# Kernel optimization log

Measured on AMD Instinct MI355X. Metric: run time of the kernel, lower is better.

Reference implementation:

```python
import jax, jax.numpy as jnp
import numpy as np

S, B, I, H, O = 512, 256, 64, 512, 25

def setup_inputs() -> dict:
    key = jax.random.key(0)
    ks = jax.random.split(key, 7)
    k = 1.0 / np.sqrt(H)  # torch nn.RNN / nn.Linear default init bound
    x = jax.random.normal(ks[0], (S, B, I), dtype=jnp.float32)
    W_ih = jax.random.uniform(ks[1], (H, I), jnp.float32, -k, k)
    W_hh = jax.random.uniform(ks[2], (H, H), jnp.float32, -k, k)
    b_ih = jax.random.uniform(ks[3], (H,), jnp.float32, -k, k)
    b_hh = jax.random.uniform(ks[4], (H,), jnp.float32, -k, k)
    W2 = jax.random.uniform(ks[5], (O, H), jnp.float32, -k, k)
    b2 = jax.random.uniform(ks[6], (O,), jnp.float32, -k, k)
    return {"x": x, "W_ih": W_ih, "W_hh": W_hh, "b_ih": b_ih, "b_hh": b_hh, "W2": W2, "b2": b2}

def reference(x, W_ih, W_hh, b_ih, b_hh, W2, b2):
    # Precompute input projection for all timesteps in one big GEMM: (S,B,H)
    xi = jnp.einsum('sbi,hi->sbh', x, W_ih) + b_ih
    h0 = jnp.zeros((x.shape[1], W_hh.shape[0]), dtype=x.dtype)
    W_hh_T = W_hh.T
    def step(h_prev, xi_t):
        h = jax.nn.relu(xi_t + h_prev @ W_hh_T + b_hh)
        return h, h
    _, out = jax.lax.scan(step, h0, xi)  # out: (S, B, H)
    # Faithful to original: out[:, -1, :] selects last batch element -> (S, H)
    y = out[:, -1, :] @ W2.T + b2  # (S, 25)
    return y
```

## Files before the change

### kernel.cpp

```cpp
#include <hip/hip_runtime.h>


#define S_ 512
#define B_ 256
#define I_ 64
#define H_ 512
#define O_ 25
#define G_ 16
#define R_ 32

__global__ __launch_bounds__(256) void rnn_pre(
    const float* __restrict__ x, const float* __restrict__ W_ih,
    const float* __restrict__ b_ih, const float* __restrict__ b_hh,
    float* __restrict__ xi, unsigned* __restrict__ hg) {
  const int t = blockIdx.x;
  const int tid = threadIdx.x;
  const int o = blockIdx.y * 256 + tid;
  if (t == 0 && blockIdx.y == 0) {
    hg[tid] = 0x80000000u;
    hg[tid + 256] = 0x80000000u;
    hg[tid + 512] = 0x80000000u;
    hg[tid + 768] = 0x80000000u;
  }
  __shared__ float xr[I_];
  if (tid < I_) xr[tid] = x[(t * B_ + (B_ - 1)) * I_ + tid];
  __syncthreads();
  float acc = b_ih[o] + b_hh[o];
  const float4* wp = (const float4*)(W_ih + o * I_);
#pragma unroll
  for (int j = 0; j < I_ / 4; ++j) {
    float4 w4 = wp[j];
    acc += w4.x * xr[4 * j] + w4.y * xr[4 * j + 1] + w4.z * xr[4 * j + 2] +
           w4.w * xr[4 * j + 3];
  }
  xi[t * H_ + o] = acc;
}

__global__ __launch_bounds__(256) void rnn_seq(
    const float* __restrict__ W_hh, const float* __restrict__ xi,
    float* __restrict__ hseq, unsigned* __restrict__ hg) {
  const int tid = threadIdx.x;
  const int b = blockIdx.x;
  const int r = tid & 31;
  const int seg = tid >> 5;
  const int row = b * R_ + r;
  const int k0 = seg * 64;
  const int wave = tid >> 6;
  const int own_lo = b * R_;
  const int own_hi = b * R_ + R_;

  __shared__ float h_l[H_];
  __shared__ float part[4 * R_];

  float w[64];
  {
    const float4* wp = (const float4*)(W_hh + row * H_ + k0);
#pragma unroll
    for (int j = 0; j < 16; ++j) {
      float4 v = wp[j];
      w[4 * j] = v.x; w[4 * j + 1] = v.y; w[4 * j + 2] = v.z; w[4 * j + 3] = v.w;
    }
  }
  for (int n = tid; n < H_; n += 256) h_l[n] = 0.0f;

  float xiv = (tid < R_) ? xi[own_lo + tid] : 0.0f;
  __syncthreads();

  const int n0 = tid, n1 = tid + 256;
  const bool own0 = (n0 >= own_lo && n0 < own_hi);
  const bool own1 = (n1 >= own_lo && n1 < own_hi);

  for (int s = 0; s < S_; ++s) {
    float a0 = 0.f, a1 = 0.f, a2 = 0.f, a3 = 0.f;
    const float4* hp = (const float4*)(h_l + k0);
#pragma unroll
    for (int j = 0; j < 16; ++j) {
      float4 hv = hp[j];
      a0 = fmaf(w[4 * j + 0], hv.x, a0);
      a1 = fmaf(w[4 * j + 1], hv.y, a1);
      a2 = fmaf(w[4 * j + 2], hv.z, a2);
      a3 = fmaf(w[4 * j + 3], hv.w, a3);
    }
    float acc = (a0 + a1) + (a2 + a3);
    acc += __shfl_xor(acc, 32, 64);
    if ((tid & 32) == 0) part[wave * R_ + r] = acc;
    __syncthreads();

    const unsigned phase = (unsigned)((s >> 1) & 1);
    unsigned* buf = hg + (s & 1) * H_;

    if (tid < R_) {
      float sum = part[tid] + part[R_ + tid] + part[2 * R_ + tid] +
                  part[3 * R_ + tid] + xiv;
      float h = fmaxf(sum, 0.0f);
      h_l[own_lo + tid] = h;
      hseq[s * H_ + own_lo + tid] = h;
      __hip_atomic_store(&buf[own_lo + tid],
                         __float_as_uint(h) | (phase << 31),
                         __ATOMIC_RELAXED, __HIP_MEMORY_SCOPE_AGENT);
    }

    if (s == S_ - 1) break;

    if (tid < R_) xiv = xi[(s + 1) * H_ + own_lo + tid];

    bool need0 = !own0, need1 = !own1;
    unsigned p0, p1;
    while (need0 | need1) {
      if (need0)
        p0 = __hip_atomic_load(&buf[n0], __ATOMIC_RELAXED, __HIP_MEMORY_SCOPE_AGENT);
      if (need1)
        p1 = __hip_atomic_load(&buf[n1], __ATOMIC_RELAXED, __HIP_MEMORY_SCOPE_AGENT);
      if (need0 && (p0 >> 31) == phase) {
        h_l[n0] = __uint_as_float(p0 & 0x7fffffffu);
        need0 = false;
      }
      if (need1 && (p1 >> 31) == phase) {
        h_l[n1] = __uint_as_float(p1 & 0x7fffffffu);
        need1 = false;
      }
    }
    __syncthreads();
  }
}

__global__ __launch_bounds__(256) void rnn_post(
    const float* __restrict__ hseq, const float* __restrict__ W2,
    const float* __restrict__ b2, float* __restrict__ y) {
  const int t = blockIdx.x;
  const int tid = threadIdx.x;
  __shared__ float hl[H_];
  __shared__ float part[256];
  for (int n = tid; n < H_; n += 256) hl[n] = hseq[t * H_ + n];
  __syncthreads();
  const int o = tid >> 3;
  const int seg = tid & 7;
  float acc = 0.0f;
  if (o < O_) {
    const float4* wp = (const float4*)(W2 + o * H_ + seg * 64);
    const float4* hp = (const float4*)(hl + seg * 64);
#pragma unroll
    for (int j = 0; j < 16; ++j) {
      float4 w4 = wp[j];
      float4 h4 = hp[j];
      acc += w4.x * h4.x + w4.y * h4.y + w4.z * h4.z + w4.w * h4.w;
    }
  }
  part[tid] = acc;
  __syncthreads();
  if (tid < O_) {
    float sum = 0.0f;
#pragma unroll
    for (int j = 0; j < 8; ++j) sum += part[tid * 8 + j];
    y[t * O_ + tid] = sum + b2[tid];
  }
}

extern "C" void kernel_launch(void* const* d_in, const int* in_sizes, int n_in,
                              void* d_out, int out_size, void* d_ws, size_t ws_size,
                              hipStream_t stream) {
  const float* x    = (const float*)d_in[0];
  const float* W_ih = (const float*)d_in[1];
  const float* W_hh = (const float*)d_in[2];
  const float* b_ih = (const float*)d_in[3];
  const float* b_hh = (const float*)d_in[4];
  const float* W2   = (const float*)d_in[5];
  const float* b2   = (const float*)d_in[6];
  float* y = (float*)d_out;

  float* xi   = (float*)d_ws;
  float* hseq = xi + S_ * H_;
  unsigned* hg = (unsigned*)(hseq + S_ * H_);

  rnn_pre<<<dim3(S_, 2), 256, 0, stream>>>(x, W_ih, b_ih, b_hh, xi, hg);
  rnn_seq<<<G_, 256, 0, stream>>>(W_hh, xi, hseq, hg);
  rnn_post<<<S_, 256, 0, stream>>>(hseq, W2, b2, y);
}
```

Before: 819.6 us.

## Halve sequential RNN blocks, use per-block mailboxes and double-buffered hidden state

Cuts the persistent recurrence kernel from 16 to 8 blocks, each owning 64 rows, with four threads per row reducing through shuffles instead of a shared-memory partial sum plus barrier. Each block now has its own mailbox, and producers push their values to every other block rather than publishing to one shared global buffer. A double-buffered shared hidden state removes one __syncthreads per step. In exchange each thread holds 128 weight registers, which risks spills, and more atomic stores are issued per step.

```diff
diff --git a/kernel.cpp b/kernel.cpp
--- a/kernel.cpp
+++ b/kernel.cpp
@@ -6,21 +6,18 @@
 #define I_ 64
 #define H_ 512
 #define O_ 25
-#define G_ 16
-#define R_ 32
+#define G_ 8
+#define R_ 64
 
 __global__ __launch_bounds__(256) void rnn_pre(
     const float* __restrict__ x, const float* __restrict__ W_ih,
     const float* __restrict__ b_ih, const float* __restrict__ b_hh,
-    float* __restrict__ xi, unsigned* __restrict__ hg) {
+    float* __restrict__ xi, unsigned* __restrict__ mbox) {
   const int t = blockIdx.x;
   const int tid = threadIdx.x;
   const int o = blockIdx.y * 256 + tid;
   if (t == 0 && blockIdx.y == 0) {
-    hg[tid] = 0x80000000u;
-    hg[tid + 256] = 0x80000000u;
-    hg[tid + 512] = 0x80000000u;
-    hg[tid + 768] = 0x80000000u;
+    for (int j = tid; j < G_ * 2 * H_; j += 256) mbox[j] = 0x80000000u;
   }
   __shared__ float xr[I_];
   if (tid < I_) xr[tid] = x[(t * B_ + (B_ - 1)) * I_ + tid];
@@ -38,43 +35,46 @@
 
 __global__ __launch_bounds__(256) void rnn_seq(
     const float* __restrict__ W_hh, const float* __restrict__ xi,
-    float* __restrict__ hseq, unsigned* __restrict__ hg) {
+    float* __restrict__ hseq, unsigned* __restrict__ mbox) {
   const int tid = threadIdx.x;
   const int b = blockIdx.x;
-  const int r = tid & 31;
-  const int seg = tid >> 5;
-  const int row = b * R_ + r;
-  const int k0 = seg * 64;
-  const int wave = tid >> 6;
+  const int row_l = tid >> 2;
+  const int q = tid & 3;
+  const int row = b * R_ + row_l;
+  const int k0 = q * 128;
   const int own_lo = b * R_;
-  const int own_hi = b * R_ + R_;
 
-  __shared__ float h_l[H_];
-  __shared__ float part[4 * R_];
+  __shared__ float h_l[2][H_];
 
-  float w[64];
+  float w[128];
   {
     const float4* wp = (const float4*)(W_hh + row * H_ + k0);
 #pragma unroll
-    for (int j = 0; j < 16; ++j) {
+    for (int j = 0; j < 32; ++j) {
       float4 v = wp[j];
       w[4 * j] = v.x; w[4 * j + 1] = v.y; w[4 * j + 2] = v.z; w[4 * j + 3] = v.w;
     }
   }
-  for (int n = tid; n < H_; n += 256) h_l[n] = 0.0f;
+  for (int n = tid; n < H_; n += 256) h_l[0][n] = 0.0f;
 
-  float xiv = (tid < R_) ? xi[own_lo + tid] : 0.0f;
+  const bool fin = (q == 0);
+  float xiv = fin ? xi[own_lo + row_l] : 0.0f;
   __syncthreads();
 
   const int n0 = tid, n1 = tid + 256;
-  const bool own0 = (n0 >= own_lo && n0 < own_hi);
-  const bool own1 = (n1 >= own_lo && n1 < own_hi);
+  const bool own0 = (n0 >= own_lo && n0 < own_lo + R_);
+  const bool own1 = (n1 >= own_lo && n1 < own_lo + R_);
+  unsigned* const mb0 = mbox + (b * 2 + 0) * H_;
+  unsigned* const mb1 = mbox + (b * 2 + 1) * H_;
 
   for (int s = 0; s < S_; ++s) {
+    const float* hr = h_l[s & 1];
+    float* hw = h_l[(s + 1) & 1];
+
     float a0 = 0.f, a1 = 0.f, a2 = 0.f, a3 = 0.f;
-    const float4* hp = (const float4*)(h_l + k0);
+    const float4* hp = (const float4*)(hr + k0);
 #pragma unroll
-    for (int j = 0; j < 16; ++j) {
+    for (int j = 0; j < 32; ++j) {
       float4 hv = hp[j];
       a0 = fmaf(w[4 * j + 0], hv.x, a0);
       a1 = fmaf(w[4 * j + 1], hv.y, a1);
@@ -82,28 +82,30 @@
       a3 = fmaf(w[4 * j + 3], hv.w, a3);
     }
     float acc = (a0 + a1) + (a2 + a3);
-    acc += __shfl_xor(acc, 32, 64);
-    if ((tid & 32) == 0) part[wave * R_ + r] = acc;
-    __syncthreads();
+    acc += __shfl_xor(acc, 1, 64);
+    acc += __shfl_xor(acc, 2, 64);
 
     const unsigned phase = (unsigned)((s >> 1) & 1);
-    unsigned* buf = hg + (s & 1) * H_;
+    const int bsel = s & 1;
 
-    if (tid < R_) {
-      float sum = part[tid] + part[R_ + tid] + part[2 * R_ + tid] +
-                  part[3 * R_ + tid] + xiv;
-      float h = fmaxf(sum, 0.0f);
-      h_l[own_lo + tid] = h;
-      hseq[s * H_ + own_lo + tid] = h;
-      __hip_atomic_store(&buf[own_lo + tid],
-                         __float_as_uint(h) | (phase << 31),
-                         __ATOMIC_RELAXED, __HIP_MEMORY_SCOPE_AGENT);
+    if (fin) {
+      float h = fmaxf(acc + xiv, 0.0f);
+      hw[row] = h;
+      hseq[s * H_ + row] = h;
+      unsigned pk = __float_as_uint(h) | (phase << 31);
+#pragma unroll
+      for (int c = 0; c < G_; ++c) {
+        if (c != b)
+          __hip_atomic_store(&mbox[(c * 2 + bsel) * H_ + row], pk,
+                             __ATOMIC_RELAXED, __HIP_MEMORY_SCOPE_AGENT);
+      }
     }
 
     if (s == S_ - 1) break;
 
-    if (tid < R_) xiv = xi[(s + 1) * H_ + own_lo + tid];
+    if (fin) xiv = xi[(s + 1) * H_ + own_lo + row_l];
 
+    unsigned* const buf = bsel ? mb1 : mb0;
     bool need0 = !own0, need1 = !own1;
     unsigned p0, p1;
     while (need0 | need1) {
@@ -112,11 +114,11 @@
       if (need1)
         p1 = __hip_atomic_load(&buf[n1], __ATOMIC_RELAXED, __HIP_MEMORY_SCOPE_AGENT);
       if (need0 && (p0 >> 31) == phase) {
-        h_l[n0] = __uint_as_float(p0 & 0x7fffffffu);
+        hw[n0] = __uint_as_float(p0 & 0x7fffffffu);
         need0 = false;
       }
       if (need1 && (p1 >> 31) == phase) {
-        h_l[n1] = __uint_as_float(p1 & 0x7fffffffu);
+        hw[n1] = __uint_as_float(p1 & 0x7fffffffu);
         need1 = false;
       }
     }
@@ -170,9 +172,9 @@
 
   float* xi   = (float*)d_ws;
   float* hseq = xi + S_ * H_;
-  unsigned* hg = (unsigned*)(hseq + S_ * H_);
+  unsigned* mbox = (unsigned*)(hseq + S_ * H_);
 
-  rnn_pre<<<dim3(S_, 2), 256, 0, stream>>>(x, W_ih, b_ih, b_hh, xi, hg);
-  rnn_seq<<<G_, 256, 0, stream>>>(W_hh, xi, hseq, hg);
+  rnn_pre<<<dim3(S_, 2), 256, 0, stream>>>(x, W_ih, b_ih, b_hh, xi, mbox);
+  rnn_seq<<<G_, 256, 0, stream>>>(W_hh, xi, hseq, mbox);
   rnn_post<<<S_, 256, 0, stream>>>(hseq, W2, b2, y);
 }
```

Result: slower. 1.096 ms (+33.7%).
